# Optimization experiments

Hardware: AMD Instinct MI355X
Metric: run time of the kernel (lower is better)

Reference implementation:

```python
import jax, jax.numpy as jnp
import numpy as np

NEG_SLOPE = 0.2  # PyG GATConv default negative_slope


def _gat_conv(h_in, src, dst, W, a_src, a_dst, b, num_nodes, heads, out_dim, concat):
    # h: [N, heads, out_dim]
    h = (h_in @ W).reshape(num_nodes, heads, out_dim)
    # per-node attention contributions: [N, heads]
    alpha_s = jnp.einsum('nhd,hd->nh', h, a_src)
    alpha_d = jnp.einsum('nhd,hd->nh', h, a_dst)
    # per-edge logits: [E, heads]
    e = jax.nn.leaky_relu(alpha_s[src] + alpha_d[dst], NEG_SLOPE)
    # segment softmax over destination nodes
    m = jax.ops.segment_max(e, dst, num_segments=num_nodes)
    m = jnp.where(jnp.isfinite(m), m, 0.0)
    e = jnp.exp(e - m[dst])
    denom = jax.ops.segment_sum(e, dst, num_segments=num_nodes)
    alpha = e / (denom[dst] + 1e-16)  # [E, heads]
    # weighted scatter-aggregate of source features
    msg = h[src] * alpha[:, :, None]  # [E, heads, out_dim]
    out = jax.ops.segment_sum(msg, dst, num_segments=num_nodes)  # [N, heads, out_dim]
    if concat:
        out = out.reshape(num_nodes, heads * out_dim)
    else:
        out = out.mean(axis=1)
    return out + b


def setup_inputs() -> dict:
    key = jax.random.key(0)
    ks = jax.random.split(key, 9)
    N, E, IN, D, H = 50000, 800000, 256, 64, 4
    x = jax.random.normal(ks[0], (N, IN), dtype=jnp.float32)
    edge_index = jax.random.randint(ks[1], (2, E), 0, N, dtype=jnp.int32)
    s = 0.06  # small init scale
    W1 = jax.random.normal(ks[2], (IN, H * D), dtype=jnp.float32) * s
    att_src1 = jax.random.normal(ks[3], (H, D), dtype=jnp.float32) * s
    att_dst1 = jax.random.normal(ks[4], (H, D), dtype=jnp.float32) * s
    b1 = jnp.zeros((H * D,), dtype=jnp.float32)
    W2 = jax.random.normal(ks[5], (H * D, D), dtype=jnp.float32) * s
    att_src2 = jax.random.normal(ks[6], (1, D), dtype=jnp.float32) * s
    att_dst2 = jax.random.normal(ks[7], (1, D), dtype=jnp.float32) * s
    b2 = jnp.zeros((D,), dtype=jnp.float32)
    return {"x": x, "edge_index": edge_index, "W1": W1, "att_src1": att_src1,
            "att_dst1": att_dst1, "b1": b1, "W2": W2, "att_src2": att_src2,
            "att_dst2": att_dst2, "b2": b2}


def reference(x, edge_index, W1, att_src1, att_dst1, b1, W2, att_src2, att_dst2, b2):
    N = x.shape[0]
    H, D = att_src1.shape
    # PyG GATConv adds self-loops by default
    loop = jnp.arange(N, dtype=edge_index.dtype)
    src = jnp.concatenate([edge_index[0], loop])
    dst = jnp.concatenate([edge_index[1], loop])
    h = _gat_conv(x, src, dst, W1, att_src1, att_dst1, b1, N, H, D, concat=True)
    h = jax.nn.relu(h)  # dropout is eval no-op
    out = _gat_conv(h, src, dst, W2, att_src2, att_dst2, b2, N, 1, D, concat=False)
    return out
```

## Files before the change

### kernel.cpp

```cpp
#include <hip/hip_runtime.h>
#include <hip/hip_bf16.h>

typedef __attribute__((ext_vector_type(8))) short short8v;
typedef __attribute__((ext_vector_type(4))) float f32x4;
typedef __attribute__((ext_vector_type(2))) float f32x2;

__device__ __forceinline__ float lrelu(float x) { return x > 0.f ? x : 0.2f * x; }
__device__ __forceinline__ ushort f2bf(float v) {
  __hip_bfloat16 b = __float2bfloat16(v);
  return *(ushort*)&b;
}
__device__ __forceinline__ float bf2f(ushort u) {
  return __uint_as_float(((unsigned)u) << 16);
}
__device__ __forceinline__ f32x2 unpk_lo_hi(unsigned u) {
  return (f32x2){__uint_as_float(u << 16), __uint_as_float(u & 0xFFFF0000u)};
}
__device__ __forceinline__ float cvtub0(unsigned u) {
  float f; asm("v_cvt_f32_ubyte0 %0, %1" : "=v"(f) : "v"(u)); return f;
}
__device__ __forceinline__ float cvtub1(unsigned u) {
  float f; asm("v_cvt_f32_ubyte1 %0, %1" : "=v"(f) : "v"(u)); return f;
}
__device__ __forceinline__ float cvtub2(unsigned u) {
  float f; asm("v_cvt_f32_ubyte2 %0, %1" : "=v"(f) : "v"(u)); return f;
}
__device__ __forceinline__ float cvtub3(unsigned u) {
  float f; asm("v_cvt_f32_ubyte3 %0, %1" : "=v"(f) : "v"(u)); return f;
}
__device__ __forceinline__ void gload16(const ushort* g, ushort* l) {
  __builtin_amdgcn_global_load_lds((const __attribute__((address_space(1))) void*)g,
                                   (__attribute__((address_space(3))) void*)l, 16, 0, 0);
}

__global__ __launch_bounds__(256) void prep_kernel(const float* __restrict__ x,
    const float* __restrict__ W1, const float* __restrict__ W2,
    const int* __restrict__ dst, ushort* __restrict__ A1, ushort* __restrict__ B1t,
    ushort* __restrict__ B2t, int* __restrict__ counts, ushort* __restrict__ rank,
    int N, int Mpad, int E, int Etot, int PX, int PW) {
  int b = blockIdx.x, t = threadIdx.x;
  if (b < PX) {
    int idx = (b * 256 + t) * 4;
    int row = idx >> 8, c = idx & 255;
    float4 v = (row < N) ? *(const float4*)&x[idx] : make_float4(0.f, 0.f, 0.f, 0.f);
    *(ushort4*)&A1[(size_t)row * 256 + c] =
        make_ushort4(f2bf(v.x), f2bf(v.y), f2bf(v.z), f2bf(v.w));
  } else if (b < PX + PW) {
    int idx = (b - PX) * 256 + t;
    if (idx < 256 * 256) {
      int k = idx >> 8, col = idx & 255;
      float v = W1[idx];
      ushort hi = f2bf(v), lo = f2bf(v - bf2f(hi));
      size_t bb = (size_t)col * 512;
      B1t[bb + k] = hi;
      B1t[bb + 256 + k] = lo;
    } else if (idx < 256 * 256 + 256 * 64) {
      int j = idx - 256 * 256;
      int k = j >> 6, col = j & 63;
      float v = W2[j];
      ushort hi = f2bf(v), lo = f2bf(v - bf2f(hi));
      size_t bb = (size_t)col * 512;
      B2t[bb + k] = hi;
      B2t[bb + 256 + k] = lo;
    }
  } else {
    int e = (b - PX - PW) * 256 + t;
    if (e < Etot) {
      int d = (e < E) ? dst[e] : (e - E);
      int r = atomicAdd(&counts[d], 1);
      rank[e] = (ushort)r;
    }
  }
}

template<int BN, int NF, int EPI, int KT, int KAT>
__global__ __launch_bounds__(256) void gemm_mfma(
    const ushort* __restrict__ A, const ushort* __restrict__ Bt,
    const float* __restrict__ avs, const float* __restrict__ avd,
    void* __restrict__ Hb, float* __restrict__ hs,
    float* __restrict__ os, float* __restrict__ od, int M, int NN) {
  constexpr int BM = 128, BK = 64;
  __shared__ ushort As[BM * BK];
  __shared__ ushort Bs[BN * BK];
  const int t = threadIdx.x, l = t & 63, w = t >> 6;
  const int l15 = l & 15, l4 = l >> 4;
  const int m0 = blockIdx.y * BM, n0 = blockIdx.x * BN;
  const int wr = w >> 1, wc = w & 1;
  f32x4 acc[4][NF];
#pragma unroll
  for (int m = 0; m < 4; ++m)
#pragma unroll
    for (int n = 0; n < NF; ++n) acc[m][n] = (f32x4){0.f, 0.f, 0.f, 0.f};

  for (int kk = 0; kk < KT; kk += BK) {
    const int ka = (kk < KAT) ? kk : kk - KAT;
    __syncthreads();
#pragma unroll
    for (int i = 0; i < 4; ++i) {
      int q = w * 4 + i;
      int c = q * 64 + l;
      int row = c >> 3, k8 = c & 7;
      int k8s = k8 ^ (row & 7);
      gload16(&A[(size_t)(m0 + row) * KAT + ka + k8s * 8], &As[q * 512]);
    }
    constexpr int BCHW = (BN * 8 / 64) / 4;
#pragma unroll
    for (int i = 0; i < BCHW; ++i) {
      int q = w * BCHW + i;
      int c = q * 64 + l;
      int col = c >> 3, k8 = c & 7;
      int k8s = k8 ^ (col & 7);
      gload16(&Bt[(size_t)(n0 + col) * KT + kk + k8s * 8], &Bs[q * 512]);
    }
    __syncthreads();
#pragma unroll
    for (int ks = 0; ks < 2; ++ks) {
      int kb = ks * 4 + l4;
      short8v af[4], bfr[NF];
#pragma unroll
      for (int m = 0; m < 4; ++m) {
        int row = wr * 64 + m * 16 + l15;
        af[m] = *(const short8v*)&As[row * 64 + (kb ^ (row & 7)) * 8];
      }
#pragma unroll
      for (int n = 0; n < NF; ++n) {
        int col = wc * (NF * 16) + n * 16 + l15;
        bfr[n] = *(const short8v*)&Bs[col * 64 + (kb ^ (col & 7)) * 8];
      }
#pragma unroll
      for (int m = 0; m < 4; ++m)
#pragma unroll
        for (int n = 0; n < NF; ++n)
          acc[m][n] = __builtin_amdgcn_mfma_f32_16x16x32_bf16(af[m], bfr[n], acc[m][n], 0, 0, 0);
    }
  }
  if (EPI == 1) {
    unsigned char* hq = (unsigned char*)Hb;
    const int head = (n0 + wc * 64) >> 6;
#pragma unroll
    for (int m = 0; m < 4; ++m) {
#pragma unroll
      for (int r = 0; r < 4; ++r) {
        int row = m0 + wr * 64 + m * 16 + l4 * 4 + r;
        float s = 0.f;
#pragma unroll
        for (int n = 0; n < NF; ++n) s = fmaxf(s, fabsf(acc[m][n][r]));
#pragma unroll
        for (int off = 1; off < 16; off <<= 1) s = fmaxf(s, __shfl_xor(s, off, 64));
        float inv = s > 0.f ? 127.f / s : 0.f;
        if (row < M) {
          unsigned char* rp = hq + (size_t)row * 256;
#pragma unroll
          for (int n = 0; n < NF; ++n) {
            int f = n * 16 + l15;
            int qv = (int)rintf(acc[m][n][r] * inv) + 128;
            rp[4 * f + head] = (unsigned char)qv;
          }
          if (l15 == 0) hs[(size_t)row * 4 + head] = s * (1.f / 127.f);
        }
      }
    }
  } else {
    ushort* hb = (ushort*)Hb;
#pragma unroll
    for (int m = 0; m < 4; ++m) {
      int rbase = m0 + wr * 64 + m * 16 + l4 * 4;
#pragma unroll
      for (int n = 0; n < NF; ++n) {
        int gcol = n0 + wc * (NF * 16) + n * 16 + l15;
#pragma unroll
        for (int r = 0; r < 4; ++r) {
          int row = rbase + r;
          if (row < M) hb[(size_t)row * NN + gcol] = f2bf(acc[m][n][r]);
        }
      }
    }
  }
  float cs[NF], cd[NF];
#pragma unroll
  for (int n = 0; n < NF; ++n) {
    int gc = n0 + wc * (NF * 16) + n * 16 + l15;
    cs[n] = avs[gc];
    cd[n] = avd[gc];
  }
  const int H = NN >> 6;
  const int head = (n0 + wc * (NF * 16)) >> 6;
#pragma unroll
  for (int m = 0; m < 4; ++m) {
#pragma unroll
    for (int r = 0; r < 4; ++r) {
      float ps = 0.f, pd = 0.f;
#pragma unroll
      for (int n = 0; n < NF; ++n) { ps += acc[m][n][r] * cs[n]; pd += acc[m][n][r] * cd[n]; }
#pragma unroll
      for (int off = 1; off < 16; off <<= 1) {
        ps += __shfl_xor(ps, off, 64);
        pd += __shfl_xor(pd, off, 64);
      }
      if (l15 == 0) {
        int row = m0 + wr * 64 + m * 16 + l4 * 4 + r;
        if (row < M) {
          if (NF == 4) {
            os[(size_t)row * H + head] = ps;
            od[(size_t)row * H + head] = pd;
          } else {
            atomicAdd(&os[row], ps);
            atomicAdd(&od[row], pd);
          }
        }
      }
    }
  }
}

static constexpr int SCB = 2048;

__global__ __launch_bounds__(256) void scan1_kernel(const int* __restrict__ counts,
    int* __restrict__ offsets, int* __restrict__ bsums, int n) {
  __shared__ int wsum[4];
  int t = threadIdx.x, lane = t & 63, w = t >> 6;
  int base = blockIdx.x * SCB + t * 8;
  int c[8];
  if (base + 7 < n) {
    int4 v0 = *(const int4*)&counts[base];
    int4 v1 = *(const int4*)&counts[base + 4];
    c[0] = v0.x; c[1] = v0.y; c[2] = v0.z; c[3] = v0.w;
    c[4] = v1.x; c[5] = v1.y; c[6] = v1.z; c[7] = v1.w;
  } else {
#pragma unroll
    for (int j = 0; j < 8; ++j) c[j] = (base + j < n) ? counts[base + j] : 0;
  }
  int ts = 0;
#pragma unroll
  for (int j = 0; j < 8; ++j) ts += c[j];
  int x = ts;
#pragma unroll
  for (int off = 1; off < 64; off <<= 1) {
    int y = __shfl_up(x, off, 64);
    if (lane >= off) x += y;
  }
  if (lane == 63) wsum[w] = x;
  __syncthreads();
  int wpre = 0;
  for (int ww = 0; ww < w; ++ww) wpre += wsum[ww];
  int ex = wpre + x - ts;
  int o[8];
#pragma unroll
  for (int j = 0; j < 8; ++j) { o[j] = ex; ex += c[j]; }
  if (base + 7 < n) {
    *(int4*)&offsets[base] = make_int4(o[0], o[1], o[2], o[3]);
    *(int4*)&offsets[base + 4] = make_int4(o[4], o[5], o[6], o[7]);
  } else {
#pragma unroll
    for (int j = 0; j < 8; ++j) if (base + j < n) offsets[base + j] = o[j];
  }
  if (t == 255) bsums[blockIdx.x] = wpre + x;
}

__global__ __launch_bounds__(256) void scan2_kernel(const int* __restrict__ bsums,
    int* __restrict__ bbase, int nb) {
  __shared__ int wsum[4];
  int t = threadIdx.x, lane = t & 63, w = t >> 6;
  int v = (t < nb) ? bsums[t] : 0;
  int x = v;
#pragma unroll
  for (int off = 1; off < 64; off <<= 1) {
    int y = __shfl_up(x, off, 64);
    if (lane >= off) x += y;
  }
  if (lane == 63) wsum[w] = x;
  __syncthreads();
  int wpre = 0;
  for (int ww = 0; ww < w; ++ww) wpre += wsum[ww];
  if (t < nb) bbase[t] = wpre + x - v;
}

__global__ __launch_bounds__(256) void scan3_kernel(int* __restrict__ offsets,
    const int* __restrict__ bbase, int n, int total) {
  int t = threadIdx.x;
  int bb = bbase[blockIdx.x];
  int base = blockIdx.x * SCB + t * 8;
  if (base + 7 < n) {
    int4 v0 = *(const int4*)&offsets[base];
    int4 v1 = *(const int4*)&offsets[base + 4];
    v0.x += bb; v0.y += bb; v0.z += bb; v0.w += bb;
    v1.x += bb; v1.y += bb; v1.z += bb; v1.w += bb;
    *(int4*)&offsets[base] = v0;
    *(int4*)&offsets[base + 4] = v1;
  } else {
#pragma unroll
    for (int j = 0; j < 8; ++j)
      if (base + j < n) offsets[base + j] += bb;
  }
  if (blockIdx.x == 0 && t == 0) offsets[n] = total;
}

__global__ __launch_bounds__(256) void scatter_kernel(const int* __restrict__ src,
    const int* __restrict__ dst, const ushort* __restrict__ rank,
    const int* __restrict__ offsets, ushort* __restrict__ src_sorted, int E, int Etot) {
  int e0 = (blockIdx.x * 256 + threadIdx.x) * 4;
  if (e0 + 3 < E) {
    int4 s4 = *(const int4*)&src[e0];
    int4 d4 = *(const int4*)&dst[e0];
    ushort4 r4 = *(const ushort4*)&rank[e0];
    src_sorted[offsets[d4.x] + r4.x] = (ushort)s4.x;
    src_sorted[offsets[d4.y] + r4.y] = (ushort)s4.y;
    src_sorted[offsets[d4.z] + r4.z] = (ushort)s4.z;
    src_sorted[offsets[d4.w] + r4.w] = (ushort)s4.w;
  } else {
#pragma unroll
    for (int j = 0; j < 4; ++j) {
      int e = e0 + j;
      if (e >= Etot) break;
      int s = (e < E) ? src[e] : (e - E);
      int d = (e < E) ? dst[e] : (e - E);
      src_sorted[offsets[d] + rank[e]] = (ushort)s;
    }
  }
}

__global__ __launch_bounds__(256) void agg1_kernel(const unsigned char* __restrict__ h1q,
    const float* __restrict__ hs, const float* __restrict__ as1,
    const float* __restrict__ ad1, const int* __restrict__ offsets,
    const ushort* __restrict__ src_sorted, const float* __restrict__ b1,
    ushort* __restrict__ A2, int N, int Mpad) {
  __shared__ float4 pl[4][64];
  __shared__ alignas(16) unsigned sl[4][64];
  int wv = threadIdx.x >> 6;
  int wid = (blockIdx.x << 2) + wv;
  int lane = threadIdx.x & 63;
  if (wid >= Mpad) return;
  size_t ab = (size_t)wid * 256;
  if (wid >= N) {
#pragma unroll
    for (int i = 0; i < 4; ++i) A2[ab + i * 64 + lane] = 0;
    return;
  }
  float4 ah = *(const float4*)&ad1[(size_t)wid * 4];
  int st = offsets[wid], en = offsets[wid + 1];
  float acc0 = 0.f, acc1 = 0.f, acc2 = 0.f, acc3 = 0.f;
  float ds0 = 0.f, ds1 = 0.f, ds2 = 0.f, ds3 = 0.f;
  float ws0 = 0.f, ws1 = 0.f, ws2 = 0.f, ws3 = 0.f;
  const unsigned lo4 = (unsigned)lane * 4;
  for (int c = st; c < en; c += 64) {
    int mye = c + lane;
    float4 w4 = make_float4(0.f, 0.f, 0.f, 0.f);
    unsigned soff = 0;
    if (mye < en) {
      int smy = (int)src_sorted[mye];
      soff = ((unsigned)smy << 8);
      float4 a4 = *(const float4*)&as1[(size_t)smy * 4];
      float4 sc4 = *(const float4*)&hs[(size_t)smy * 4];
      float p0 = __expf(lrelu(a4.x + ah.x));
      float p1 = __expf(lrelu(a4.y + ah.y));
      float p2 = __expf(lrelu(a4.z + ah.z));
      float p3 = __expf(lrelu(a4.w + ah.w));
      ds0 += p0; ds1 += p1; ds2 += p2; ds3 += p3;
      w4 = make_float4(p0 * sc4.x, p1 * sc4.y, p2 * sc4.z, p3 * sc4.w);
      ws0 += w4.x; ws1 += w4.y; ws2 += w4.z; ws3 += w4.w;
    }
    pl[wv][lane] = w4;
    sl[wv][lane] = soff;
    int cnt = min(64, en - c);
    int e = 0;
    for (; e + 4 <= cnt; e += 4) {
      uint4 s4 = *(const uint4*)&sl[wv][e];
      float4 w0 = pl[wv][e + 0];
      float4 w1 = pl[wv][e + 1];
      float4 w2 = pl[wv][e + 2];
      float4 w3 = pl[wv][e + 3];
      unsigned u0 = *(const unsigned*)(h1q + (s4.x + lo4));
      unsigned u1 = *(const unsigned*)(h1q + (s4.y + lo4));
      unsigned u2 = *(const unsigned*)(h1q + (s4.z + lo4));
      unsigned u3 = *(const unsigned*)(h1q + (s4.w + lo4));
      acc0 = fmaf(w0.x, cvtub0(u0), acc0); acc1 = fmaf(w0.y, cvtub1(u0), acc1);
      acc2 = fmaf(w0.z, cvtub2(u0), acc2); acc3 = fmaf(w0.w, cvtub3(u0), acc3);
      acc0 = fmaf(w1.x, cvtub0(u1), acc0); acc1 = fmaf(w1.y, cvtub1(u1), acc1);
      acc2 = fmaf(w1.z, cvtub2(u1), acc2); acc3 = fmaf(w1.w, cvtub3(u1), acc3);
      acc0 = fmaf(w2.x, cvtub0(u2), acc0); acc1 = fmaf(w2.y, cvtub1(u2), acc1);
      acc2 = fmaf(w2.z, cvtub2(u2), acc2); acc3 = fmaf(w2.w, cvtub3(u2), acc3);
      acc0 = fmaf(w3.x, cvtub0(u3), acc0); acc1 = fmaf(w3.y, cvtub1(u3), acc1);
      acc2 = fmaf(w3.z, cvtub2(u3), acc2); acc3 = fmaf(w3.w, cvtub3(u3), acc3);
    }
    for (; e < cnt; ++e) {
      unsigned sb = sl[wv][e];
      float4 w4e = pl[wv][e];
      unsigned u = *(const unsigned*)(h1q + (sb + lo4));
      acc0 = fmaf(w4e.x, cvtub0(u), acc0); acc1 = fmaf(w4e.y, cvtub1(u), acc1);
      acc2 = fmaf(w4e.z, cvtub2(u), acc2); acc3 = fmaf(w4e.w, cvtub3(u), acc3);
    }
  }
#pragma unroll
  for (int off = 32; off > 0; off >>= 1) {
    ds0 += __shfl_xor(ds0, off, 64);
    ds1 += __shfl_xor(ds1, off, 64);
    ds2 += __shfl_xor(ds2, off, 64);
    ds3 += __shfl_xor(ds3, off, 64);
    ws0 += __shfl_xor(ws0, off, 64);
    ws1 += __shfl_xor(ws1, off, 64);
    ws2 += __shfl_xor(ws2, off, 64);
    ws3 += __shfl_xor(ws3, off, 64);
  }
  float v[4];
  v[0] = fmaxf((acc0 - 128.f * ws0) / (ds0 + 1e-16f) + b1[lane], 0.f);
  v[1] = fmaxf((acc1 - 128.f * ws1) / (ds1 + 1e-16f) + b1[64 + lane], 0.f);
  v[2] = fmaxf((acc2 - 128.f * ws2) / (ds2 + 1e-16f) + b1[128 + lane], 0.f);
  v[3] = fmaxf((acc3 - 128.f * ws3) / (ds3 + 1e-16f) + b1[192 + lane], 0.f);
#pragma unroll
  for (int h = 0; h < 4; ++h) A2[ab + h * 64 + lane] = f2bf(v[h]);
}

__global__ __launch_bounds__(256) void agg2_kernel(const ushort* __restrict__ h2b,
    const float* __restrict__ as2, const float* __restrict__ ad2,
    const int* __restrict__ offsets, const ushort* __restrict__ src_sorted,
    const float* __restrict__ b2, float* __restrict__ out, int N) {
  __shared__ float pl[4][64];
  __shared__ alignas(16) int sl[4][64];
  int wv = threadIdx.x >> 6;
  int wid = (blockIdx.x << 2) + wv;
  int lane = threadIdx.x & 63;
  if (wid >= N) return;
  const int qtr = lane >> 4;
  const int fl = lane & 15;
  float ah = ad2[wid];
  int st = offsets[wid], en = offsets[wid + 1];
  f32x2 a01 = (f32x2){0.f, 0.f}, a23 = (f32x2){0.f, 0.f};
  float ds = 0.f;
  for (int c = st; c < en; c += 64) {
    int mye = c + lane;
    float p = 0.f;
    int smy = 0;
    if (mye < en) {
      smy = (int)src_sorted[mye];
      p = __expf(lrelu(as2[smy] + ah));
    }
    ds += p;
    pl[wv][lane] = p;
    sl[wv][lane] = smy;
    int cnt = min(64, en - c);
    for (int e = 0; e < cnt; e += 4) {
      int e2 = e + qtr;
      int row = sl[wv][e2];
      float q = pl[wv][e2];
      uint2 u = *(const uint2*)&h2b[(size_t)row * 64 + fl * 4];
      a01 += (f32x2){q, q} * unpk_lo_hi(u.x);
      a23 += (f32x2){q, q} * unpk_lo_hi(u.y);
    }
  }
#pragma unroll
  for (int off = 32; off > 0; off >>= 1) ds += __shfl_xor(ds, off, 64);
#pragma unroll
  for (int off = 16; off <= 32; off <<= 1) {
    a01.x += __shfl_xor(a01.x, off, 64);
    a01.y += __shfl_xor(a01.y, off, 64);
    a23.x += __shfl_xor(a23.x, off, 64);
    a23.y += __shfl_xor(a23.y, off, 64);
  }
  if (lane < 16) {
    float inv = 1.f / (ds + 1e-16f);
    float4 bb = *(const float4*)&b2[fl * 4];
    float4 o;
    o.x = a01.x * inv + bb.x;
    o.y = a01.y * inv + bb.y;
    o.z = a23.x * inv + bb.z;
    o.w = a23.y * inv + bb.w;
    *(float4*)&out[(size_t)wid * 64 + fl * 4] = o;
  }
}

extern "C" void kernel_launch(void* const* d_in, const int* in_sizes, int n_in,
                              void* d_out, int out_size, void* d_ws, size_t ws_size,
                              hipStream_t stream) {
  const float* x      = (const float*)d_in[0];
  const int*   ei     = (const int*)d_in[1];
  const float* W1     = (const float*)d_in[2];
  const float* a_src1 = (const float*)d_in[3];
  const float* a_dst1 = (const float*)d_in[4];
  const float* b1     = (const float*)d_in[5];
  const float* W2     = (const float*)d_in[6];
  const float* a_src2 = (const float*)d_in[7];
  const float* a_dst2 = (const float*)d_in[8];
  const float* b2     = (const float*)d_in[9];
  float* out = (float*)d_out;

  const int IN = 256, HD = 256, D2 = 64;
  const int N = in_sizes[0] / IN;
  const int E = in_sizes[1] / 2;
  const int Etot = E + N;
  const int Mpad = ((N + 127) / 128) * 128;
  const int* srcp = ei;
  const int* dstp = ei + E;

  uintptr_t base = (uintptr_t)d_ws;
  auto alloc_bytes = [&](size_t nbytes) -> void* {
    void* p = (void*)base;
    base += (nbytes + 255) & ~(size_t)255;
    return p;
  };
  ushort* A1        = (ushort*)alloc_bytes((size_t)Mpad * 256 * 2);
  ushort* A2        = (ushort*)alloc_bytes((size_t)Mpad * 256 * 2);
  unsigned char* h1q = (unsigned char*)alloc_bytes((size_t)N * 256);
  float* hs         = (float*)alloc_bytes((size_t)N * 4 * 4);
  ushort* h2b       = (ushort*)alloc_bytes((size_t)N * D2 * 2);
  ushort* B1t       = (ushort*)alloc_bytes((size_t)HD * 512 * 2);
  ushort* B2t       = (ushort*)alloc_bytes((size_t)D2 * 512 * 2);
  float* as1        = (float*)alloc_bytes((size_t)N * 4 * 4);
  float* ad1        = (float*)alloc_bytes((size_t)N * 4 * 4);
  float* as2        = (float*)alloc_bytes((size_t)N * 4);
  float* ad2        = (float*)alloc_bytes((size_t)N * 4);
  int* counts       = (int*)alloc_bytes((size_t)(N + 1) * 4);
  uintptr_t zero_end = base;
  int* offsets      = (int*)alloc_bytes((size_t)(N + 1) * 4);
  ushort* rank      = (ushort*)alloc_bytes((size_t)Etot * 2);
  ushort* src_sorted = (ushort*)alloc_bytes((size_t)Etot * 2);
  int* bsums        = (int*)alloc_bytes(256 * 4);
  int* bbase        = (int*)alloc_bytes(256 * 4);

  hipMemsetAsync((void*)as2, 0, zero_end - (uintptr_t)as2, stream);

  const int nwb  = (N + 3) / 4;
  const int nwbp = (Mpad + 3) / 4;
  const int neb  = (Etot + 255) / 256;
  const int nsb  = (N + SCB - 1) / SCB;
  const int PX = Mpad / 4;
  const int PW = (256 * 256 + 256 * 64) / 256;

  prep_kernel<<<PX + PW + neb, 256, 0, stream>>>(x, W1, W2, dstp, A1, B1t, B2t,
                                                 counts, rank, N, Mpad, E, Etot, PX, PW);
  scan1_kernel<<<nsb, 256, 0, stream>>>(counts, offsets, bsums, N);
  scan2_kernel<<<1, 256, 0, stream>>>(bsums, bbase, nsb);
  scan3_kernel<<<nsb, 256, 0, stream>>>(offsets, bbase, N, Etot);
  scatter_kernel<<<(Etot + 1023) / 1024, 256, 0, stream>>>(srcp, dstp, rank, offsets,
                                                           src_sorted, E, Etot);
  gemm_mfma<128, 4, 1, 512, 256><<<dim3(HD / 128, Mpad / 128), 256, 0, stream>>>(
      A1, B1t, a_src1, a_dst1, (void*)h1q, hs, as1, ad1, N, HD);
  agg1_kernel<<<nwbp, 256, 0, stream>>>(h1q, hs, as1, ad1, offsets, src_sorted, b1, A2, N, Mpad);
  gemm_mfma<64, 2, 0, 512, 256><<<dim3(D2 / 64, Mpad / 128), 256, 0, stream>>>(
      A2, B2t, a_src2, a_dst2, (void*)h2b, nullptr, as2, ad2, N, D2);
  agg2_kernel<<<nwb, 256, 0, stream>>>(h2b, as2, ad2, offsets, src_sorted, b2, out, N);
}
```

Measured before the change: 207.2 us.

## Replace global-atomic counting sort with two-pass LDS radix bucketing by destination

Edge sorting by destination moves from per-edge global atomics (counts and rank) plus a scatter to a two-level radix scheme. A block histogram on the high byte of dst is followed by a scan over the histogram matrix and a scatter into coarse buckets of packed (dst, src) words. A per-bucket pass then sorts on the low byte with LDS atomics and writes offsets and src_sorted. This removes contended global atomics and the rank array. In exchange it adds an extra intermediate buffer pass, a larger scan, and a final pass with only about 200 blocks.

```diff
diff --git a/kernel.cpp b/kernel.cpp
--- a/kernel.cpp
+++ b/kernel.cpp
@@ -35,9 +35,8 @@
 
 __global__ __launch_bounds__(256) void prep_kernel(const float* __restrict__ x,
     const float* __restrict__ W1, const float* __restrict__ W2,
-    const int* __restrict__ dst, ushort* __restrict__ A1, ushort* __restrict__ B1t,
-    ushort* __restrict__ B2t, int* __restrict__ counts, ushort* __restrict__ rank,
-    int N, int Mpad, int E, int Etot, int PX, int PW) {
+    ushort* __restrict__ A1, ushort* __restrict__ B1t, ushort* __restrict__ B2t,
+    int N, int Mpad, int PX) {
   int b = blockIdx.x, t = threadIdx.x;
   if (b < PX) {
     int idx = (b * 256 + t) * 4;
@@ -45,7 +44,7 @@
     float4 v = (row < N) ? *(const float4*)&x[idx] : make_float4(0.f, 0.f, 0.f, 0.f);
     *(ushort4*)&A1[(size_t)row * 256 + c] =
         make_ushort4(f2bf(v.x), f2bf(v.y), f2bf(v.z), f2bf(v.w));
-  } else if (b < PX + PW) {
+  } else {
     int idx = (b - PX) * 256 + t;
     if (idx < 256 * 256) {
       int k = idx >> 8, col = idx & 255;
@@ -63,14 +62,77 @@
       B2t[bb + k] = hi;
       B2t[bb + 256 + k] = lo;
     }
-  } else {
-    int e = (b - PX - PW) * 256 + t;
-    if (e < Etot) {
-      int d = (e < E) ? dst[e] : (e - E);
-      int r = atomicAdd(&counts[d], 1);
-      rank[e] = (ushort)r;
-    }
-  }
+  }
+}
+
+static constexpr int RCH = 2048;
+
+__global__ __launch_bounds__(256) void histA_kernel(const int* __restrict__ dst,
+    int* __restrict__ histmat, int E, int Etot, int NBA) {
+  __shared__ int h[256];
+  int t = threadIdx.x, b = blockIdx.x;
+  h[t] = 0;
+  __syncthreads();
+  int s0 = b * RCH, s1 = min(s0 + RCH, Etot);
+  for (int e = s0 + t; e < s1; e += 256) {
+    int d = (e < E) ? dst[e] : (e - E);
+    atomicAdd(&h[d >> 8], 1);
+  }
+  __syncthreads();
+  histmat[t * NBA + b] = h[t];
+}
+
+__global__ __launch_bounds__(256) void scatterA_kernel(const int* __restrict__ src,
+    const int* __restrict__ dst, const int* __restrict__ histscan,
+    unsigned* __restrict__ bufA, int E, int Etot, int NBA) {
+  __shared__ int cur[256];
+  int t = threadIdx.x, b = blockIdx.x;
+  cur[t] = histscan[t * NBA + b];
+  __syncthreads();
+  int s0 = b * RCH, s1 = min(s0 + RCH, Etot);
+  for (int e = s0 + t; e < s1; e += 256) {
+    int s = (e < E) ? src[e] : (e - E);
+    int d = (e < E) ? dst[e] : (e - E);
+    int pos = atomicAdd(&cur[d >> 8], 1);
+    bufA[pos] = ((unsigned)d << 16) | (unsigned)s;
+  }
+}
+
+__global__ __launch_bounds__(256) void passB_kernel(const unsigned* __restrict__ bufA,
+    const int* __restrict__ histscan, ushort* __restrict__ src_sorted,
+    int* __restrict__ offsets, int N, int Etot, int NBA, int NHB) {
+  __shared__ int hist[256], cur[256], wsum[4];
+  int t = threadIdx.x, hb = blockIdx.x;
+  int base = histscan[(size_t)hb * NBA];
+  int bend = (hb + 1 < NHB) ? histscan[(size_t)(hb + 1) * NBA] : Etot;
+  hist[t] = 0;
+  __syncthreads();
+  for (int i = base + t; i < bend; i += 256)
+    atomicAdd(&hist[(bufA[i] >> 16) & 255], 1);
+  __syncthreads();
+  int lane = t & 63, w = t >> 6;
+  int v = hist[t];
+  int x = v;
+#pragma unroll
+  for (int off = 1; off < 64; off <<= 1) {
+    int y = __shfl_up(x, off, 64);
+    if (lane >= off) x += y;
+  }
+  if (lane == 63) wsum[w] = x;
+  __syncthreads();
+  int wpre = 0;
+  for (int ww = 0; ww < w; ++ww) wpre += wsum[ww];
+  int ex = wpre + x - v;
+  cur[t] = base + ex;
+  int d = hb * 256 + t;
+  if (d < N) offsets[d] = base + ex;
+  __syncthreads();
+  for (int i = base + t; i < bend; i += 256) {
+    unsigned k = bufA[i];
+    int pos = atomicAdd(&cur[(k >> 16) & 255], 1);
+    src_sorted[pos] = (ushort)(k & 0xFFFFu);
+  }
+  if (hb == 0 && t == 0) offsets[N] = Etot;
 }
 
 template<int BN, int NF, int EPI, int KT, int KAT>
@@ -293,30 +355,6 @@
       if (base + j < n) offsets[base + j] += bb;
   }
   if (blockIdx.x == 0 && t == 0) offsets[n] = total;
-}
-
-__global__ __launch_bounds__(256) void scatter_kernel(const int* __restrict__ src,
-    const int* __restrict__ dst, const ushort* __restrict__ rank,
-    const int* __restrict__ offsets, ushort* __restrict__ src_sorted, int E, int Etot) {
-  int e0 = (blockIdx.x * 256 + threadIdx.x) * 4;
-  if (e0 + 3 < E) {
-    int4 s4 = *(const int4*)&src[e0];
-    int4 d4 = *(const int4*)&dst[e0];
-    ushort4 r4 = *(const ushort4*)&rank[e0];
-    src_sorted[offsets[d4.x] + r4.x] = (ushort)s4.x;
-    src_sorted[offsets[d4.y] + r4.y] = (ushort)s4.y;
-    src_sorted[offsets[d4.z] + r4.z] = (ushort)s4.z;
-    src_sorted[offsets[d4.w] + r4.w] = (ushort)s4.w;
-  } else {
-#pragma unroll
-    for (int j = 0; j < 4; ++j) {
-      int e = e0 + j;
-      if (e >= Etot) break;
-      int s = (e < E) ? src[e] : (e - E);
-      int d = (e < E) ? dst[e] : (e - E);
-      src_sorted[offsets[d] + rank[e]] = (ushort)s;
-    }
-  }
 }
 
 __global__ __launch_bounds__(256) void agg1_kernel(const unsigned char* __restrict__ h1q,
@@ -490,6 +528,9 @@
   const int Mpad = ((N + 127) / 128) * 128;
   const int* srcp = ei;
   const int* dstp = ei + E;
+  const int NBA = (Etot + RCH - 1) / RCH;
+  const int NHB = (N + 255) / 256;
+  const int NH  = NBA * 256;
 
   uintptr_t base = (uintptr_t)d_ws;
   auto alloc_bytes = [&](size_t nbytes) -> void* {
@@ -508,11 +549,12 @@
   float* ad1        = (float*)alloc_bytes((size_t)N * 4 * 4);
   float* as2        = (float*)alloc_bytes((size_t)N * 4);
   float* ad2        = (float*)alloc_bytes((size_t)N * 4);
-  int* counts       = (int*)alloc_bytes((size_t)(N + 1) * 4);
   uintptr_t zero_end = base;
   int* offsets      = (int*)alloc_bytes((size_t)(N + 1) * 4);
-  ushort* rank      = (ushort*)alloc_bytes((size_t)Etot * 2);
   ushort* src_sorted = (ushort*)alloc_bytes((size_t)Etot * 2);
+  unsigned* bufA    = (unsigned*)alloc_bytes((size_t)Etot * 4);
+  int* histmat      = (int*)alloc_bytes((size_t)(NH + 1) * 4);
+  int* histscan     = (int*)alloc_bytes((size_t)(NH + 1) * 4);
   int* bsums        = (int*)alloc_bytes(256 * 4);
   int* bbase        = (int*)alloc_bytes(256 * 4);
 
@@ -520,18 +562,18 @@
 
   const int nwb  = (N + 3) / 4;
   const int nwbp = (Mpad + 3) / 4;
-  const int neb  = (Etot + 255) / 256;
-  const int nsb  = (N + SCB - 1) / SCB;
+  const int nsbA = (NH + SCB - 1) / SCB;
   const int PX = Mpad / 4;
   const int PW = (256 * 256 + 256 * 64) / 256;
 
-  prep_kernel<<<PX + PW + neb, 256, 0, stream>>>(x, W1, W2, dstp, A1, B1t, B2t,
-                                                 counts, rank, N, Mpad, E, Etot, PX, PW);
-  scan1_kernel<<<nsb, 256, 0, stream>>>(counts, offsets, bsums, N);
-  scan2_kernel<<<1, 256, 0, stream>>>(bsums, bbase, nsb);
-  scan3_kernel<<<nsb, 256, 0, stream>>>(offsets, bbase, N, Etot);
-  scatter_kernel<<<(Etot + 1023) / 1024, 256, 0, stream>>>(srcp, dstp, rank, offsets,
-                                                           src_sorted, E, Etot);
+  prep_kernel<<<PX + PW, 256, 0, stream>>>(x, W1, W2, A1, B1t, B2t, N, Mpad, PX);
+  histA_kernel<<<NBA, 256, 0, stream>>>(dstp, histmat, E, Etot, NBA);
+  scan1_kernel<<<nsbA, 256, 0, stream>>>(histmat, histscan, bsums, NH);
+  scan2_kernel<<<1, 256, 0, stream>>>(bsums, bbase, nsbA);
+  scan3_kernel<<<nsbA, 256, 0, stream>>>(histscan, bbase, NH, Etot);
+  scatterA_kernel<<<NBA, 256, 0, stream>>>(srcp, dstp, histscan, bufA, E, Etot, NBA);
+  passB_kernel<<<NHB, 256, 0, stream>>>(bufA, histscan, src_sorted, offsets,
+                                        N, Etot, NBA, NHB);
   gemm_mfma<128, 4, 1, 512, 256><<<dim3(HD / 128, Mpad / 128), 256, 0, stream>>>(
       A1, B1t, a_src1, a_dst1, (void*)h1q, hs, as1, ad1, N, HD);
   agg1_kernel<<<nwbp, 256, 0, stream>>>(h1q, hs, as1, ad1, offsets, src_sorted, b1, A2, N, Mpad);
```

Result: faster. 187.8 us (median of 2 runs) (-9.4%).
